# Performance work log

Hardware: AMD Instinct MI355X
Metric: run time of the kernel (lower is better)

The kernel has to match this reference:

```python
import jax, jax.numpy as jnp
import numpy as np

L_MAX = 3
N_RADIAL = [2, 2, 1, 1]  # radial powers r^{2k} with 2k+l <= l_max=3


def fibonacci_sphere(n):
    i = np.arange(n, dtype=np.float64)
    phi = np.pi * (3.0 - np.sqrt(5.0))
    y = 1.0 - 2.0 * i / (n - 1)
    r = np.sqrt(np.maximum(1.0 - y * y, 0.0))
    th = phi * i
    pts = np.stack([np.cos(th) * r, y, np.sin(th) * r], -1)
    return jnp.asarray(pts, dtype=jnp.float32)


def real_sh(u):
    # real spherical harmonics on unit vectors u[...,3], degrees 0..3
    x, y, z = u[..., 0], u[..., 1], u[..., 2]
    Y0 = 0.28209479 * jnp.ones_like(x)[..., None]
    Y1 = 0.48860251 * jnp.stack([y, z, x], -1)
    Y2 = jnp.stack([
        1.09254843 * x * y,
        1.09254843 * y * z,
        0.31539157 * (3.0 * z * z - 1.0),
        1.09254843 * x * z,
        0.54627421 * (x * x - y * y)], -1)
    Y3 = jnp.stack([
        0.59004359 * y * (3.0 * x * x - y * y),
        2.89061144 * x * y * z,
        0.45704579 * y * (5.0 * z * z - 1.0),
        0.37317633 * z * (5.0 * z * z - 3.0),
        0.45704579 * x * (5.0 * z * z - 1.0),
        1.44530572 * z * (x * x - y * y),
        0.59004359 * x * (x * x - 3.0 * y * y)], -1)
    return [Y0, Y1, Y2, Y3]


def grid_sample_3d(vol, grid):
    # vol: [B, D, H, W]; grid: [B, d, h, w, 3], grid[...,0]->W, [...,1]->H, [...,2]->D
    # align_corners=True, zeros padding (torch.nn.functional.grid_sample semantics)
    B, Dv, Hv, Wv = vol.shape
    ix = (grid[..., 0] + 1.0) * 0.5 * (Wv - 1)
    iy = (grid[..., 1] + 1.0) * 0.5 * (Hv - 1)
    iz = (grid[..., 2] + 1.0) * 0.5 * (Dv - 1)
    x0f, y0f, z0f = jnp.floor(ix), jnp.floor(iy), jnp.floor(iz)
    wx, wy, wz = ix - x0f, iy - y0f, iz - z0f
    x0, y0, z0 = x0f.astype(jnp.int32), y0f.astype(jnp.int32), z0f.astype(jnp.int32)
    x1, y1, z1 = x0 + 1, y0 + 1, z0 + 1
    bidx = jnp.arange(B).reshape(B, 1, 1, 1)

    def tap(zi, yi, xi):
        m = ((zi >= 0) & (zi < Dv) & (yi >= 0) & (yi < Hv) & (xi >= 0) & (xi < Wv)).astype(vol.dtype)
        v = vol[bidx, jnp.clip(zi, 0, Dv - 1), jnp.clip(yi, 0, Hv - 1), jnp.clip(xi, 0, Wv - 1)]
        return v * m

    out = (tap(z0, y0, x0) * (1 - wz) * (1 - wy) * (1 - wx)
         + tap(z0, y0, x1) * (1 - wz) * (1 - wy) * wx
         + tap(z0, y1, x0) * (1 - wz) * wy * (1 - wx)
         + tap(z0, y1, x1) * (1 - wz) * wy * wx
         + tap(z1, y0, x0) * wz * (1 - wy) * (1 - wx)
         + tap(z1, y0, x1) * wz * (1 - wy) * wx
         + tap(z1, y1, x0) * wz * wy * (1 - wx)
         + tap(z1, y1, x1) * wz * wy * wx)
    return out


def setup_inputs() -> dict:
    key = jax.random.key(0)
    ks = jax.random.split(key, 12)
    B, H, W, D, S = 8, 32, 32, 32, 64
    x = jax.random.normal(ks[0], (B, H, W, D, 3), jnp.float32) * 0.35
    x_density = jax.random.uniform(ks[1], (B, H, W, D), jnp.float32)
    F = jax.random.normal(ks[2], (B, S, 256), jnp.float32) * 0.1
    def lin(k, i, o):
        return jax.random.normal(k, (i, o), jnp.float32) / np.sqrt(i)
    return {
        'x': x, 'x_density': x_density, 'F': F,
        'S2': fibonacci_sphere(S),
        'bw1': lin(ks[3], 256, 64), 'bb1': jnp.zeros((64,), jnp.float32),
        'bw2': lin(ks[4], 64, 3), 'bb2': jnp.zeros((3,), jnp.float32),
        'cw1': lin(ks[5], 256, 128), 'cb1': jnp.zeros((128,), jnp.float32),
        'cw2': lin(ks[6], 128, 64), 'cb2': jnp.zeros((64,), jnp.float32),
        'iw': lin(ks[7], 128, 3), 'ib': jnp.zeros((3,), jnp.float32),
    }


def reference(x, x_density, F, S2, bw1, bb1, bw2, bb2, cw1, cb1, cw2, cb2, iw, ib):
    B, H, W, D, _ = x.shape
    S = S2.shape[0]
    quad = (4.0 * jnp.pi) / S  # sphere quadrature weight for fibonacci samples
    Ybase = real_sh(S2)  # list of [S, 2l+1]

    # frame (E) branch: basis MLP -> type-1 SH coefficients -> normalize
    basis = jax.nn.relu(F @ bw1 + bb1) @ bw2 + bb2          # [B,S,3]
    E = jnp.einsum('vm,bvc->bmc', Ybase[1], basis) * quad   # [B,3,3]
    E = E / jnp.clip(jnp.linalg.norm(E, axis=-1, keepdims=True), 1e-6)

    # latent code branch: code MLP -> full SHT coefficients per degree l
    latent = jax.nn.relu(F @ cw1 + cb1) @ cw2 + cb2         # [B,S,64]
    coeffs = [jnp.einsum('vm,bvc->bmc', Ybase[l], latent) * quad for l in range(L_MAX + 1)]

    # zernike monomials of the grid points
    xf = x.reshape(B, -1, 3)                                # [B,V,3]
    r = jnp.linalg.norm(xf, axis=-1, keepdims=True)         # [B,V,1]
    u = xf / jnp.clip(r, 1e-6)
    Yx = real_sh(u)
    points_code = []
    points_inv = None
    for l in range(L_MAX + 1):
        Pl = Yx[l] * (r ** l)                               # solid harmonic [B,V,2l+1]
        rad = jnp.stack([r[..., 0] ** (2 * k) for k in range(N_RADIAL[l])], -1)  # [B,V,n_l]
        zl = Pl[..., :, None] * rad[..., None, :]           # [B,V,2l+1,n_l]
        p = jnp.einsum('bmi,bvmj->bvij', coeffs[l], zl)     # [B,V,64,n_l]
        p = p.reshape(B, p.shape[1], -1)
        points_code.append(p)
        if l == 1:
            points_inv = p                                  # [B,V,128]
    points_code = jnp.concatenate(points_code, -1)          # [B,V,384]

    pts = points_inv @ iw + ib                              # [B,V,3]
    coords = pts.reshape(B, H, W, D, 3)
    vol = x_density.reshape(B, H, W, D)
    sampled = grid_sample_3d(vol, coords)                   # [B,H,W,D]
    return sampled, E, coords, points_code
```

## Files before the change

kernel.cpp:

```cpp
#include <hip/hip_runtime.h>
#include <math.h>

#define OFF_E     262144
#define OFF_COORD 262216
#define OFF_CODE  1048648

#define QUAD 0.19634954084936207f

#define WS_H1 0
#define WS_H2 32768
#define WS_C  98304
#define WS_AB 106496

__global__ __launch_bounds__(384) void k_hidden(
    const float* __restrict__ F,
    const float* __restrict__ bw1, const float* __restrict__ bb1,
    const float* __restrict__ cw1, const float* __restrict__ cb1,
    float* __restrict__ ws)
{
    __shared__ float sF[8 * 257];
    const int blk = blockIdx.x;
    const int b   = blk >> 3;
    const int r0  = (blk & 7) * 8;
    const int tid = threadIdx.x;

    float* wsH1 = ws + WS_H1;
    float* wsH2 = ws + WS_H2;

    const float* Fb = F + ((size_t)b * 64 + r0) * 256;
    for (int i = tid; i < 2048; i += 384) sF[(i >> 8) * 257 + (i & 255)] = Fb[i];
    __syncthreads();

    if (tid < 128) {
        const int row = tid >> 4, k4 = (tid & 15) * 4;
        const float* fr = sF + row * 257;
        float4 acc = *(const float4*)&bb1[k4];
        #pragma unroll 4
        for (int j = 0; j < 256; ++j) {
            const float  f = fr[j];
            const float4 w = *(const float4*)&bw1[j * 64 + k4];
            acc.x = fmaf(f, w.x, acc.x);
            acc.y = fmaf(f, w.y, acc.y);
            acc.z = fmaf(f, w.z, acc.z);
            acc.w = fmaf(f, w.w, acc.w);
        }
        acc.x = fmaxf(acc.x, 0.f); acc.y = fmaxf(acc.y, 0.f);
        acc.z = fmaxf(acc.z, 0.f); acc.w = fmaxf(acc.w, 0.f);
        *(float4*)&wsH1[((size_t)b * 64 + r0 + row) * 64 + k4] = acc;
    } else {
        const int tt  = tid - 128;
        const int row = tt >> 5, k4 = (tt & 31) * 4;
        const float* fr = sF + row * 257;
        float4 acc = *(const float4*)&cb1[k4];
        #pragma unroll 4
        for (int j = 0; j < 256; ++j) {
            const float  f = fr[j];
            const float4 w = *(const float4*)&cw1[j * 128 + k4];
            acc.x = fmaf(f, w.x, acc.x);
            acc.y = fmaf(f, w.y, acc.y);
            acc.z = fmaf(f, w.z, acc.z);
            acc.w = fmaf(f, w.w, acc.w);
        }
        acc.x = fmaxf(acc.x, 0.f); acc.y = fmaxf(acc.y, 0.f);
        acc.z = fmaxf(acc.z, 0.f); acc.w = fmaxf(acc.w, 0.f);
        *(float4*)&wsH2[((size_t)b * 64 + r0 + row) * 128 + k4] = acc;
    }
}

__global__ __launch_bounds__(512) void k_coeffs(
    const float* __restrict__ ws_in,
    const float* __restrict__ S2,
    const float* __restrict__ bw2, const float* __restrict__ bb2,
    const float* __restrict__ cw2, const float* __restrict__ cb2,
    const float* __restrict__ iw,
    float* __restrict__ ws_out, float* __restrict__ outE)
{
    __shared__ float sH2[64 * 129];
    __shared__ alignas(16) float sLat[64 * 64];
    __shared__ float sY[64 * 16];
    __shared__ float sBas[64 * 3];
    __shared__ float sC[16 * 64];
    __shared__ float sE[9];

    const int b = blockIdx.x, tid = threadIdx.x;
    const float* wsH1 = ws_in + WS_H1;
    const float* wsH2 = ws_in + WS_H2;
    float* wsC  = ws_out + WS_C;
    float* wsAB = ws_out + WS_AB;

    const float* H2b = wsH2 + (size_t)b * 8192;
    for (int i = tid; i < 8192; i += 512) sH2[(i >> 7) * 129 + (i & 127)] = H2b[i];

    if (tid < 64) {
        const float x = S2[tid * 3 + 0], y = S2[tid * 3 + 1], z = S2[tid * 3 + 2];
        float* Yv = sY + tid * 16;
        Yv[0]  = 0.28209479f;
        Yv[1]  = 0.48860251f * y;
        Yv[2]  = 0.48860251f * z;
        Yv[3]  = 0.48860251f * x;
        Yv[4]  = 1.09254843f * x * y;
        Yv[5]  = 1.09254843f * y * z;
        Yv[6]  = 0.31539157f * (3.f * z * z - 1.f);
        Yv[7]  = 1.09254843f * x * z;
        Yv[8]  = 0.54627421f * (x * x - y * y);
        Yv[9]  = 0.59004359f * y * (3.f * x * x - y * y);
        Yv[10] = 2.89061144f * x * y * z;
        Yv[11] = 0.45704579f * y * (5.f * z * z - 1.f);
        Yv[12] = 0.37317633f * z * (5.f * z * z - 3.f);
        Yv[13] = 0.45704579f * x * (5.f * z * z - 1.f);
        Yv[14] = 1.44530572f * z * (x * x - y * y);
        Yv[15] = 0.59004359f * x * (x * x - 3.f * y * y);
    }

    float breg = 0.f;
    if (tid < 192) {
        const int v = tid / 3, c = tid % 3;
        const float* h1 = wsH1 + ((size_t)b * 64 + v) * 64;
        float acc = bb2[c];
        #pragma unroll 8
        for (int k = 0; k < 64; ++k) acc = fmaf(h1[k], bw2[k * 3 + c], acc);
        breg = acc;
    }
    __syncthreads();

    if (tid < 192) sBas[tid] = breg;

    for (int t = tid; t < 1024; t += 512) {
        const int row = t >> 4, i4 = (t & 15) * 4;
        const float* h2 = sH2 + row * 129;
        float4 acc = *(const float4*)&cb2[i4];
        #pragma unroll 4
        for (int k = 0; k < 128; ++k) {
            const float  h = h2[k];
            const float4 w = *(const float4*)&cw2[k * 64 + i4];
            acc.x = fmaf(h, w.x, acc.x);
            acc.y = fmaf(h, w.y, acc.y);
            acc.z = fmaf(h, w.z, acc.z);
            acc.w = fmaf(h, w.w, acc.w);
        }
        *(float4*)&sLat[row * 64 + i4] = acc;
    }
    __syncthreads();

    for (int o = tid; o < 1024; o += 512) {
        const int m = o >> 6, i = o & 63;
        float acc = 0.f;
        #pragma unroll 8
        for (int v = 0; v < 64; ++v) acc = fmaf(sY[v * 16 + m], sLat[v * 64 + i], acc);
        acc *= QUAD;
        sC[o] = acc;
        wsC[(size_t)b * 1024 + o] = acc;
    }
    if (tid < 9) {
        const int m = tid / 3, c = tid % 3;
        float acc = 0.f;
        for (int v = 0; v < 64; ++v) acc = fmaf(sY[v * 16 + 1 + m], sBas[v * 3 + c], acc);
        sE[tid] = acc * QUAD;
    }
    __syncthreads();

    if (tid < 9) {
        const int m = tid / 3;
        const float e0 = sE[m * 3 + 0], e1 = sE[m * 3 + 1], e2 = sE[m * 3 + 2];
        const float n = sqrtf(e0 * e0 + e1 * e1 + e2 * e2);
        outE[b * 9 + tid] = sE[tid] / fmaxf(n, 1e-6f);
    }
    if (tid < 18) {
        const int which = tid / 9, mc = tid % 9;
        const int m = mc / 3, c = mc % 3;
        float acc = 0.f;
        #pragma unroll 8
        for (int i = 0; i < 64; ++i)
            acc = fmaf(sC[(1 + m) * 64 + i], iw[(2 * i + which) * 3 + c], acc);
        wsAB[b * 18 + tid] = acc;
    }
}

__global__ __launch_bounds__(384) void k_points(
    const float* __restrict__ x, const float* __restrict__ dens,
    const float* __restrict__ ws, const float* __restrict__ ib,
    float* __restrict__ out)
{
    __shared__ alignas(16) float sC[16 * 64];
    __shared__ float sAB[18];
    __shared__ alignas(16) float sZ[128 * 20];

    const int blk = blockIdx.x;
    const int b   = blk >> 8;
    const int v0  = (blk & 255) * 128;
    const int tid = threadIdx.x;

    const float* wsC  = ws + WS_C;
    const float* wsAB = ws + WS_AB;

    if (tid < 256) ((float4*)sC)[tid] = ((const float4*)(wsC + (size_t)b * 1024))[tid];
    if (tid < 18) sAB[tid] = wsAB[b * 18 + tid];

    float z1 = 0.f, z2 = 0.f, z3 = 0.f, r2 = 0.f;
    size_t g = 0;
    if (tid < 128) {
        const int v = v0 + tid;
        g = (size_t)b * 32768 + v;
        const float px = x[g * 3 + 0], py = x[g * 3 + 1], pz = x[g * 3 + 2];
        r2 = px * px + py * py + pz * pz;
        const float r   = sqrtf(r2);
        const float inv = 1.f / fmaxf(r, 1e-6f);
        const float ux = px * inv, uy = py * inv, uz = pz * inv;
        float* Z = sZ + tid * 20;
        z1 = 0.48860251f * uy * r;
        z2 = 0.48860251f * uz * r;
        z3 = 0.48860251f * ux * r;
        Z[0] = z1; Z[1] = z2; Z[2] = z3; Z[3] = r2;
        const float r3 = r2 * r;
        Z[4]  = 0.59004359f * uy * (3.f * ux * ux - uy * uy) * r3;
        Z[5]  = 2.89061144f * ux * uy * uz * r3;
        Z[6]  = 0.45704579f * uy * (5.f * uz * uz - 1.f) * r3;
        Z[7]  = 0.37317633f * uz * (5.f * uz * uz - 3.f) * r3;
        Z[8]  = 0.45704579f * ux * (5.f * uz * uz - 1.f) * r3;
        Z[9]  = 1.44530572f * uz * (ux * ux - uy * uy) * r3;
        Z[10] = 0.59004359f * ux * (ux * ux - 3.f * uy * uy) * r3;
        Z[12] = 1.09254843f * ux * uy * r2;
        Z[13] = 1.09254843f * uy * uz * r2;
        Z[14] = 0.31539157f * (3.f * uz * uz - 1.f) * r2;
        Z[15] = 1.09254843f * ux * uz * r2;
        Z[16] = 0.54627421f * (ux * ux - uy * uy) * r2;
    }
    __syncthreads();

    const int c = tid;
    float* po = out + OFF_CODE + ((size_t)b * 32768 + v0) * 384 + c;
    if (c < 128) {
        const float cr = sC[c >> 1] * 0.28209479f;
        const bool  jr = (c & 1) != 0;
        #pragma unroll 4
        for (int v = 0; v < 128; ++v) {
            const float r2v = sZ[v * 20 + 3];
            const float a = jr ? cr * r2v : cr;
            po[(size_t)v * 384] = a;
        }
    } else if (c < 256) {
        const int  i  = (c - 128) >> 1;
        const bool jr = (c & 1) != 0;
        const float c0 = sC[1 * 64 + i], c1 = sC[2 * 64 + i], c2 = sC[3 * 64 + i];
        #pragma unroll 4
        for (int v = 0; v < 128; ++v) {
            const float4 z = *(const float4*)(sZ + v * 20);
            float a = c0 * z.x;
            a = fmaf(c1, z.y, a);
            a = fmaf(c2, z.z, a);
            a = jr ? a * z.w : a;
            po[(size_t)v * 384] = a;
        }
    } else if (c < 320) {
        const int i = c - 256;
        const float c0 = sC[4 * 64 + i], c1 = sC[5 * 64 + i], c2 = sC[6 * 64 + i];
        const float c3 = sC[7 * 64 + i], c4 = sC[8 * 64 + i];
        #pragma unroll 4
        for (int v = 0; v < 128; ++v) {
            const float4 z  = *(const float4*)(sZ + v * 20 + 12);
            const float  z4 = sZ[v * 20 + 16];
            float a = c0 * z.x;
            a = fmaf(c1, z.y, a);
            a = fmaf(c2, z.z, a);
            a = fmaf(c3, z.w, a);
            a = fmaf(c4, z4,  a);
            po[(size_t)v * 384] = a;
        }
    } else {
        const int i = c - 320;
        const float c0 = sC[ 9 * 64 + i], c1 = sC[10 * 64 + i], c2 = sC[11 * 64 + i];
        const float c3 = sC[12 * 64 + i], c4 = sC[13 * 64 + i], c5 = sC[14 * 64 + i];
        const float c6 = sC[15 * 64 + i];
        #pragma unroll 4
        for (int v = 0; v < 128; ++v) {
            const float4 za = *(const float4*)(sZ + v * 20 + 4);
            const float2 zb = *(const float2*)(sZ + v * 20 + 8);
            const float  zc = sZ[v * 20 + 10];
            float a = c0 * za.x;
            a = fmaf(c1, za.y, a);
            a = fmaf(c2, za.z, a);
            a = fmaf(c3, za.w, a);
            a = fmaf(c4, zb.x, a);
            a = fmaf(c5, zb.y, a);
            a = fmaf(c6, zc,  a);
            po[(size_t)v * 384] = a;
        }
    }

    if (tid < 128) {
        const float zr0 = z1, zr1 = z2, zr2 = z3;
        float pt[3];
        #pragma unroll
        for (int cc = 0; cc < 3; ++cc) {
            float acc = ib[cc];
            acc = fmaf(zr0, sAB[0 * 3 + cc] + r2 * sAB[9 + 0 * 3 + cc], acc);
            acc = fmaf(zr1, sAB[1 * 3 + cc] + r2 * sAB[9 + 1 * 3 + cc], acc);
            acc = fmaf(zr2, sAB[2 * 3 + cc] + r2 * sAB[9 + 2 * 3 + cc], acc);
            pt[cc] = acc;
            out[OFF_COORD + g * 3 + cc] = acc;
        }

        const float ix = (pt[0] + 1.f) * 0.5f * 31.f;
        const float iy = (pt[1] + 1.f) * 0.5f * 31.f;
        const float iz = (pt[2] + 1.f) * 0.5f * 31.f;
        const float x0f = floorf(ix), y0f = floorf(iy), z0f = floorf(iz);
        const float wx = ix - x0f, wy = iy - y0f, wz = iz - z0f;
        const int x0 = (int)x0f, y0 = (int)y0f, z0 = (int)z0f;
        const float* volb = dens + (size_t)b * 32768;
        float s = 0.f;
        #pragma unroll
        for (int dz = 0; dz < 2; ++dz) {
            const int zi = z0 + dz;
            const float wzz = dz ? wz : 1.f - wz;
            #pragma unroll
            for (int dy = 0; dy < 2; ++dy) {
                const int yi = y0 + dy;
                const float wyy = dy ? wy : 1.f - wy;
                #pragma unroll
                for (int dx = 0; dx < 2; ++dx) {
                    const int xi = x0 + dx;
                    const float wxx = dx ? wx : 1.f - wx;
                    if (zi >= 0 && zi < 32 && yi >= 0 && yi < 32 && xi >= 0 && xi < 32)
                        s += wzz * wyy * wxx * volb[zi * 1024 + yi * 32 + xi];
                }
            }
        }
        out[g] = s;
    }
}

extern "C" void kernel_launch(void* const* d_in, const int* in_sizes, int n_in,
                              void* d_out, int out_size, void* d_ws, size_t ws_size,
                              hipStream_t stream) {
    const float* x    = (const float*)d_in[0];
    const float* dens = (const float*)d_in[1];
    const float* F    = (const float*)d_in[2];
    const float* S2   = (const float*)d_in[3];
    const float* bw1  = (const float*)d_in[4];
    const float* bb1  = (const float*)d_in[5];
    const float* bw2  = (const float*)d_in[6];
    const float* bb2  = (const float*)d_in[7];
    const float* cw1  = (const float*)d_in[8];
    const float* cb1  = (const float*)d_in[9];
    const float* cw2  = (const float*)d_in[10];
    const float* cb2  = (const float*)d_in[11];
    const float* iw   = (const float*)d_in[12];
    const float* ib   = (const float*)d_in[13];
    float* out = (float*)d_out;
    float* ws  = (float*)d_ws;

    k_hidden<<<64,   384, 0, stream>>>(F, bw1, bb1, cw1, cb1, ws);
    k_coeffs<<<8,    512, 0, stream>>>(ws, S2, bw2, bb2, cw2, cb2, iw, ws, out + OFF_E);
    k_points<<<2048, 384, 0, stream>>>(x, dens, ws, ib, out);
}
```

Before: 588.0 us.

## Write points_code with float4 stores by remapping threads to column groups

Restructures the output stage of the points_code kernel so each thread computes four adjacent output columns for a quarter of the vertex rows and writes them as one float4 store. Previously each thread wrote one scalar column across all 128 rows. The goal is wider, more efficient global stores for the large code output, which is likely the dominant memory traffic. The cost is more registers per thread for coefficient arrays and a different per-wave write pattern, and the l=2 and l=3 sections now use only 64 threads each with four columns apiece.

```diff
diff --git a/kernel.cpp b/kernel.cpp
--- a/kernel.cpp
+++ b/kernel.cpp
@@ -227,63 +227,95 @@
     }
     __syncthreads();
 
-    const int c = tid;
-    float* po = out + OFF_CODE + ((size_t)b * 32768 + v0) * 384 + c;
-    if (c < 128) {
-        const float cr = sC[c >> 1] * 0.28209479f;
-        const bool  jr = (c & 1) != 0;
-        #pragma unroll 4
-        for (int v = 0; v < 128; ++v) {
-            const float r2v = sZ[v * 20 + 3];
-            const float a = jr ? cr * r2v : cr;
-            po[(size_t)v * 384] = a;
-        }
-    } else if (c < 256) {
-        const int  i  = (c - 128) >> 1;
-        const bool jr = (c & 1) != 0;
-        const float c0 = sC[1 * 64 + i], c1 = sC[2 * 64 + i], c2 = sC[3 * 64 + i];
-        #pragma unroll 4
-        for (int v = 0; v < 128; ++v) {
-            const float4 z = *(const float4*)(sZ + v * 20);
-            float a = c0 * z.x;
-            a = fmaf(c1, z.y, a);
-            a = fmaf(c2, z.z, a);
-            a = jr ? a * z.w : a;
-            po[(size_t)v * 384] = a;
-        }
-    } else if (c < 320) {
-        const int i = c - 256;
-        const float c0 = sC[4 * 64 + i], c1 = sC[5 * 64 + i], c2 = sC[6 * 64 + i];
-        const float c3 = sC[7 * 64 + i], c4 = sC[8 * 64 + i];
-        #pragma unroll 4
-        for (int v = 0; v < 128; ++v) {
-            const float4 z  = *(const float4*)(sZ + v * 20 + 12);
-            const float  z4 = sZ[v * 20 + 16];
-            float a = c0 * z.x;
-            a = fmaf(c1, z.y, a);
-            a = fmaf(c2, z.z, a);
-            a = fmaf(c3, z.w, a);
-            a = fmaf(c4, z4,  a);
-            po[(size_t)v * 384] = a;
+    const size_t rowbase = OFF_CODE + ((size_t)b * 32768 + v0) * 384;
+    if (tid < 128) {
+        const int q = tid & 31, vh = tid >> 5;
+        const float ca = sC[2 * q]     * 0.28209479f;
+        const float cb = sC[2 * q + 1] * 0.28209479f;
+        const float* zr = sZ + (vh * 32) * 20 + 3;
+        float* po = out + rowbase + (size_t)(vh * 32) * 384 + 4 * q;
+        #pragma unroll 4
+        for (int vi = 0; vi < 32; ++vi) {
+            const float r2v = zr[(size_t)vi * 20];
+            float4 o;
+            o.x = ca; o.y = ca * r2v; o.z = cb; o.w = cb * r2v;
+            *(float4*)po = o;
+            po += 384;
+        }
+    } else if (tid < 256) {
+        const int u = tid - 128, q = u & 31, vh = u >> 5;
+        const float c00 = sC[64 + 2 * q],     c01 = sC[128 + 2 * q],     c02 = sC[192 + 2 * q];
+        const float c10 = sC[64 + 2 * q + 1], c11 = sC[128 + 2 * q + 1], c12 = sC[192 + 2 * q + 1];
+        const float* zr = sZ + (vh * 32) * 20;
+        float* po = out + rowbase + (size_t)(vh * 32) * 384 + 128 + 4 * q;
+        #pragma unroll 4
+        for (int vi = 0; vi < 32; ++vi) {
+            const float4 z = *(const float4*)(zr + (size_t)vi * 20);
+            float d0 = c00 * z.x; d0 = fmaf(c01, z.y, d0); d0 = fmaf(c02, z.z, d0);
+            float d1 = c10 * z.x; d1 = fmaf(c11, z.y, d1); d1 = fmaf(c12, z.z, d1);
+            float4 o;
+            o.x = d0; o.y = d0 * z.w; o.z = d1; o.w = d1 * z.w;
+            *(float4*)po = o;
+            po += 384;
+        }
+    } else if (tid < 320) {
+        const int ln = tid & 63, q = ln & 15, vh = ln >> 4;
+        const int i0 = 4 * q;
+        float cf[5][4];
+        #pragma unroll
+        for (int m = 0; m < 5; ++m)
+            #pragma unroll
+            for (int k = 0; k < 4; ++k) cf[m][k] = sC[(4 + m) * 64 + i0 + k];
+        const float* zr = sZ + (vh * 32) * 20;
+        float* po = out + rowbase + (size_t)(vh * 32) * 384 + 256 + i0;
+        #pragma unroll 4
+        for (int vi = 0; vi < 32; ++vi) {
+            const float4 za = *(const float4*)(zr + (size_t)vi * 20 + 12);
+            const float  zb = zr[(size_t)vi * 20 + 16];
+            float4 o;
+            float* a = &o.x;
+            #pragma unroll
+            for (int k = 0; k < 4; ++k) {
+                float acc = cf[0][k] * za.x;
+                acc = fmaf(cf[1][k], za.y, acc);
+                acc = fmaf(cf[2][k], za.z, acc);
+                acc = fmaf(cf[3][k], za.w, acc);
+                acc = fmaf(cf[4][k], zb,   acc);
+                a[k] = acc;
+            }
+            *(float4*)po = o;
+            po += 384;
         }
     } else {
-        const int i = c - 320;
-        const float c0 = sC[ 9 * 64 + i], c1 = sC[10 * 64 + i], c2 = sC[11 * 64 + i];
-        const float c3 = sC[12 * 64 + i], c4 = sC[13 * 64 + i], c5 = sC[14 * 64 + i];
-        const float c6 = sC[15 * 64 + i];
-        #pragma unroll 4
-        for (int v = 0; v < 128; ++v) {
-            const float4 za = *(const float4*)(sZ + v * 20 + 4);
-            const float2 zb = *(const float2*)(sZ + v * 20 + 8);
-            const float  zc = sZ[v * 20 + 10];
-            float a = c0 * za.x;
-            a = fmaf(c1, za.y, a);
-            a = fmaf(c2, za.z, a);
-            a = fmaf(c3, za.w, a);
-            a = fmaf(c4, zb.x, a);
-            a = fmaf(c5, zb.y, a);
-            a = fmaf(c6, zc,  a);
-            po[(size_t)v * 384] = a;
+        const int ln = tid & 63, q = ln & 15, vh = ln >> 4;
+        const int i0 = 4 * q;
+        float cf[7][4];
+        #pragma unroll
+        for (int m = 0; m < 7; ++m)
+            #pragma unroll
+            for (int k = 0; k < 4; ++k) cf[m][k] = sC[(9 + m) * 64 + i0 + k];
+        const float* zr = sZ + (vh * 32) * 20;
+        float* po = out + rowbase + (size_t)(vh * 32) * 384 + 320 + i0;
+        #pragma unroll 2
+        for (int vi = 0; vi < 32; ++vi) {
+            const float4 za = *(const float4*)(zr + (size_t)vi * 20 + 4);
+            const float2 zb = *(const float2*)(zr + (size_t)vi * 20 + 8);
+            const float  zc = zr[(size_t)vi * 20 + 10];
+            float4 o;
+            float* a = &o.x;
+            #pragma unroll
+            for (int k = 0; k < 4; ++k) {
+                float acc = cf[0][k] * za.x;
+                acc = fmaf(cf[1][k], za.y, acc);
+                acc = fmaf(cf[2][k], za.z, acc);
+                acc = fmaf(cf[3][k], za.w, acc);
+                acc = fmaf(cf[4][k], zb.x, acc);
+                acc = fmaf(cf[5][k], zb.y, acc);
+                acc = fmaf(cf[6][k], zc,   acc);
+                a[k] = acc;
+            }
+            *(float4*)po = o;
+            po += 384;
         }
     }
 
```

Result: faster. 556.5 us (-5.4%).

## Restructure point-code kernel for vectorized float4 stores and smaller blocks

Applied to the files above, without the earlier changes.

The points kernel is rewritten so each thread produces four consecutive code channels and writes them with a single 16-byte vector store. It uses a padded per-point monomial table in shared memory with uniform per-segment coefficient vectors, instead of one scalar store per thread per point. Blocks now cover 64 points (4096 blocks) with a batch-interleaved block index, and the coordinate and grid-sample work runs on 64 threads before the sync. This targets the store throughput of the large 384-wide code output, at the cost of some redundant multiplies by zero padding.

```diff
diff --git a/kernel.cpp b/kernel.cpp
--- a/kernel.cpp
+++ b/kernel.cpp
@@ -11,6 +11,8 @@
 #define WS_H2 32768
 #define WS_C  98304
 #define WS_AB 106496
+
+typedef float f4v __attribute__((ext_vector_type(4)));
 
 __global__ __launch_bounds__(384) void k_hidden(
     const float* __restrict__ F,
@@ -176,135 +178,74 @@
     }
 }
 
-__global__ __launch_bounds__(384) void k_points(
+__global__ __launch_bounds__(384) void k_code(
     const float* __restrict__ x, const float* __restrict__ dens,
     const float* __restrict__ ws, const float* __restrict__ ib,
     float* __restrict__ out)
 {
-    __shared__ alignas(16) float sC[16 * 64];
-    __shared__ float sAB[18];
-    __shared__ alignas(16) float sZ[128 * 20];
-
-    const int blk = blockIdx.x;
-    const int b   = blk >> 8;
-    const int v0  = (blk & 255) * 128;
-    const int tid = threadIdx.x;
-
-    const float* wsC  = ws + WS_C;
-    const float* wsAB = ws + WS_AB;
-
-    if (tid < 256) ((float4*)sC)[tid] = ((const float4*)(wsC + (size_t)b * 1024))[tid];
-    if (tid < 18) sAB[tid] = wsAB[b * 18 + tid];
-
-    float z1 = 0.f, z2 = 0.f, z3 = 0.f, r2 = 0.f;
-    size_t g = 0;
-    if (tid < 128) {
-        const int v = v0 + tid;
-        g = (size_t)b * 32768 + v;
-        const float px = x[g * 3 + 0], py = x[g * 3 + 1], pz = x[g * 3 + 2];
-        r2 = px * px + py * py + pz * pz;
+    __shared__ alignas(16) float sC[1024];
+    __shared__ alignas(16) float sT[64 * 32];
+
+    const int blk   = blockIdx.x;
+    const int b     = blk & 7;
+    const int vbase = (blk >> 3) * 64;
+    const int tid   = threadIdx.x;
+
+    if (tid < 256)
+        ((f4v*)sC)[tid] = ((const f4v*)(ws + WS_C + b * 1024))[tid];
+
+    if (tid < 64) {
+        const int g = b * 32768 + vbase + tid;
+        const float px = x[(size_t)g * 3 + 0];
+        const float py = x[(size_t)g * 3 + 1];
+        const float pz = x[(size_t)g * 3 + 2];
+        const float r2 = px * px + py * py + pz * pz;
         const float r   = sqrtf(r2);
         const float inv = 1.f / fmaxf(r, 1e-6f);
         const float ux = px * inv, uy = py * inv, uz = pz * inv;
-        float* Z = sZ + tid * 20;
-        z1 = 0.48860251f * uy * r;
-        z2 = 0.48860251f * uz * r;
-        z3 = 0.48860251f * ux * r;
-        Z[0] = z1; Z[1] = z2; Z[2] = z3; Z[3] = r2;
         const float r3 = r2 * r;
-        Z[4]  = 0.59004359f * uy * (3.f * ux * ux - uy * uy) * r3;
-        Z[5]  = 2.89061144f * ux * uy * uz * r3;
-        Z[6]  = 0.45704579f * uy * (5.f * uz * uz - 1.f) * r3;
-        Z[7]  = 0.37317633f * uz * (5.f * uz * uz - 3.f) * r3;
-        Z[8]  = 0.45704579f * ux * (5.f * uz * uz - 1.f) * r3;
-        Z[9]  = 1.44530572f * uz * (ux * ux - uy * uy) * r3;
-        Z[10] = 0.59004359f * ux * (ux * ux - 3.f * uy * uy) * r3;
-        Z[12] = 1.09254843f * ux * uy * r2;
-        Z[13] = 1.09254843f * uy * uz * r2;
-        Z[14] = 0.31539157f * (3.f * uz * uz - 1.f) * r2;
-        Z[15] = 1.09254843f * ux * uz * r2;
-        Z[16] = 0.54627421f * (ux * ux - uy * uy) * r2;
-    }
-    __syncthreads();
-
-    const int c = tid;
-    float* po = out + OFF_CODE + ((size_t)b * 32768 + v0) * 384 + c;
-    if (c < 128) {
-        const float cr = sC[c >> 1] * 0.28209479f;
-        const bool  jr = (c & 1) != 0;
-        #pragma unroll 4
-        for (int v = 0; v < 128; ++v) {
-            const float r2v = sZ[v * 20 + 3];
-            const float a = jr ? cr * r2v : cr;
-            po[(size_t)v * 384] = a;
-        }
-    } else if (c < 256) {
-        const int  i  = (c - 128) >> 1;
-        const bool jr = (c & 1) != 0;
-        const float c0 = sC[1 * 64 + i], c1 = sC[2 * 64 + i], c2 = sC[3 * 64 + i];
-        #pragma unroll 4
-        for (int v = 0; v < 128; ++v) {
-            const float4 z = *(const float4*)(sZ + v * 20);
-            float a = c0 * z.x;
-            a = fmaf(c1, z.y, a);
-            a = fmaf(c2, z.z, a);
-            a = jr ? a * z.w : a;
-            po[(size_t)v * 384] = a;
-        }
-    } else if (c < 320) {
-        const int i = c - 256;
-        const float c0 = sC[4 * 64 + i], c1 = sC[5 * 64 + i], c2 = sC[6 * 64 + i];
-        const float c3 = sC[7 * 64 + i], c4 = sC[8 * 64 + i];
-        #pragma unroll 4
-        for (int v = 0; v < 128; ++v) {
-            const float4 z  = *(const float4*)(sZ + v * 20 + 12);
-            const float  z4 = sZ[v * 20 + 16];
-            float a = c0 * z.x;
-            a = fmaf(c1, z.y, a);
-            a = fmaf(c2, z.z, a);
-            a = fmaf(c3, z.w, a);
-            a = fmaf(c4, z4,  a);
-            po[(size_t)v * 384] = a;
-        }
-    } else {
-        const int i = c - 320;
-        const float c0 = sC[ 9 * 64 + i], c1 = sC[10 * 64 + i], c2 = sC[11 * 64 + i];
-        const float c3 = sC[12 * 64 + i], c4 = sC[13 * 64 + i], c5 = sC[14 * 64 + i];
-        const float c6 = sC[15 * 64 + i];
-        #pragma unroll 4
-        for (int v = 0; v < 128; ++v) {
-            const float4 za = *(const float4*)(sZ + v * 20 + 4);
-            const float2 zb = *(const float2*)(sZ + v * 20 + 8);
-            const float  zc = sZ[v * 20 + 10];
-            float a = c0 * za.x;
-            a = fmaf(c1, za.y, a);
-            a = fmaf(c2, za.z, a);
-            a = fmaf(c3, za.w, a);
-            a = fmaf(c4, zb.x, a);
-            a = fmaf(c5, zb.y, a);
-            a = fmaf(c6, zc,  a);
-            po[(size_t)v * 384] = a;
-        }
-    }
-
-    if (tid < 128) {
-        const float zr0 = z1, zr1 = z2, zr2 = z3;
+
+        const float z1 = 0.48860251f * uy * r;
+        const float z2 = 0.48860251f * uz * r;
+        const float z3 = 0.48860251f * ux * r;
+
+        float* T = sT + tid * 32;
+        T[0]  = 1.f;  T[1] = r2;  T[2] = 0.f; T[3] = 0.f;
+        T[4]  = 0.f;  T[5] = 0.f; T[6] = 0.f; T[7] = 0.f;
+        T[8]  = z1;   T[9] = z2;  T[10] = z3;
+        T[11] = z1 * r2; T[12] = z2 * r2; T[13] = z3 * r2;
+        T[14] = 0.f;  T[15] = 0.f;
+        T[16] = 1.09254843f * ux * uy * r2;
+        T[17] = 1.09254843f * uy * uz * r2;
+        T[18] = 0.31539157f * (3.f * uz * uz - 1.f) * r2;
+        T[19] = 1.09254843f * ux * uz * r2;
+        T[20] = 0.54627421f * (ux * ux - uy * uy) * r2;
+        T[21] = 0.f; T[22] = 0.f; T[23] = 0.f;
+        T[24] = 0.59004359f * uy * (3.f * ux * ux - uy * uy) * r3;
+        T[25] = 2.89061144f * ux * uy * uz * r3;
+        T[26] = 0.45704579f * uy * (5.f * uz * uz - 1.f) * r3;
+        T[27] = 0.37317633f * uz * (5.f * uz * uz - 3.f) * r3;
+        T[28] = 0.45704579f * ux * (5.f * uz * uz - 1.f) * r3;
+        T[29] = 1.44530572f * uz * (ux * ux - uy * uy) * r3;
+        T[30] = 0.59004359f * ux * (ux * ux - 3.f * uy * uy) * r3;
+        T[31] = 0.f;
+
+        const float* AB = ws + WS_AB + b * 18;
         float pt[3];
         #pragma unroll
         for (int cc = 0; cc < 3; ++cc) {
             float acc = ib[cc];
-            acc = fmaf(zr0, sAB[0 * 3 + cc] + r2 * sAB[9 + 0 * 3 + cc], acc);
-            acc = fmaf(zr1, sAB[1 * 3 + cc] + r2 * sAB[9 + 1 * 3 + cc], acc);
-            acc = fmaf(zr2, sAB[2 * 3 + cc] + r2 * sAB[9 + 2 * 3 + cc], acc);
+            acc = fmaf(z1, AB[0 + cc] + r2 * AB[9  + cc], acc);
+            acc = fmaf(z2, AB[3 + cc] + r2 * AB[12 + cc], acc);
+            acc = fmaf(z3, AB[6 + cc] + r2 * AB[15 + cc], acc);
             pt[cc] = acc;
-            out[OFF_COORD + g * 3 + cc] = acc;
-        }
-
-        const float ix = (pt[0] + 1.f) * 0.5f * 31.f;
-        const float iy = (pt[1] + 1.f) * 0.5f * 31.f;
-        const float iz = (pt[2] + 1.f) * 0.5f * 31.f;
-        const float x0f = floorf(ix), y0f = floorf(iy), z0f = floorf(iz);
-        const float wx = ix - x0f, wy = iy - y0f, wz = iz - z0f;
+            out[OFF_COORD + (size_t)g * 3 + cc] = acc;
+        }
+        const float ixf = (pt[0] + 1.f) * 0.5f * 31.f;
+        const float iyf = (pt[1] + 1.f) * 0.5f * 31.f;
+        const float izf = (pt[2] + 1.f) * 0.5f * 31.f;
+        const float x0f = floorf(ixf), y0f = floorf(iyf), z0f = floorf(izf);
+        const float wx = ixf - x0f, wy = iyf - y0f, wz = izf - z0f;
         const int x0 = (int)x0f, y0 = (int)y0f, z0 = (int)z0f;
         const float* volb = dens + (size_t)b * 32768;
         float s = 0.f;
@@ -327,6 +268,71 @@
         }
         out[g] = s;
     }
+    __syncthreads();
+
+    const int w  = tid >> 6, l = tid & 63;
+    const int g0 = w * 256 + 4 * l;
+    const int rw = g0 / 384;
+    const int c  = g0 - rw * 384;
+
+    f4v cf0 = {0.f,0.f,0.f,0.f}, cf1 = cf0, cf2 = cf0, cf3 = cf0;
+    f4v cf4 = cf0, cf5 = cf0, cf6 = cf0;
+    int tb;
+    if (c < 128) {
+        const int i0 = c >> 1;
+        const float ca = sC[i0]     * 0.28209479f;
+        const float cb = sC[i0 + 1] * 0.28209479f;
+        cf0 = (f4v){ca, 0.f, cb, 0.f};
+        cf1 = (f4v){0.f, ca, 0.f, cb};
+        tb = 0;
+    } else if (c < 256) {
+        const int u = (c - 128) >> 1;
+        const float a0 = sC[64 + u],     a1 = sC[128 + u],     a2 = sC[192 + u];
+        const float b0 = sC[64 + u + 1], b1 = sC[128 + u + 1], b2 = sC[192 + u + 1];
+        cf0 = (f4v){a0, 0.f, b0, 0.f};
+        cf1 = (f4v){a1, 0.f, b1, 0.f};
+        cf2 = (f4v){a2, 0.f, b2, 0.f};
+        cf3 = (f4v){0.f, a0, 0.f, b0};
+        cf4 = (f4v){0.f, a1, 0.f, b1};
+        cf5 = (f4v){0.f, a2, 0.f, b2};
+        tb = 8;
+    } else if (c < 320) {
+        const int i0 = c - 256;
+        cf0 = *(const f4v*)&sC[4 * 64 + i0];
+        cf1 = *(const f4v*)&sC[5 * 64 + i0];
+        cf2 = *(const f4v*)&sC[6 * 64 + i0];
+        cf3 = *(const f4v*)&sC[7 * 64 + i0];
+        cf4 = *(const f4v*)&sC[8 * 64 + i0];
+        tb = 16;
+    } else {
+        const int i0 = c - 320;
+        cf0 = *(const f4v*)&sC[ 9 * 64 + i0];
+        cf1 = *(const f4v*)&sC[10 * 64 + i0];
+        cf2 = *(const f4v*)&sC[11 * 64 + i0];
+        cf3 = *(const f4v*)&sC[12 * 64 + i0];
+        cf4 = *(const f4v*)&sC[13 * 64 + i0];
+        cf5 = *(const f4v*)&sC[14 * 64 + i0];
+        cf6 = *(const f4v*)&sC[15 * 64 + i0];
+        tb = 24;
+    }
+
+    const float* Tb = sT + tb;
+    float* po = out + OFF_CODE + ((size_t)(b * 32768 + vbase)) * 384 + g0;
+
+    #pragma unroll 4
+    for (int p = 0; p < 16; ++p) {
+        const int ro = (4 * p + rw) * 32;
+        const f4v ta = *(const f4v*)(Tb + ro);
+        const f4v tb4 = *(const f4v*)(Tb + ro + 4);
+        f4v acc = cf0 * ta.x;
+        acc += cf1 * ta.y;
+        acc += cf2 * ta.z;
+        acc += cf3 * ta.w;
+        acc += cf4 * tb4.x;
+        acc += cf5 * tb4.y;
+        acc += cf6 * tb4.z;
+        *(f4v*)(po + p * 1536) = acc;
+    }
 }
 
 extern "C" void kernel_launch(void* const* d_in, const int* in_sizes, int n_in,
@@ -351,5 +357,5 @@
 
     k_hidden<<<64,   384, 0, stream>>>(F, bw1, bb1, cw1, cb1, ws);
     k_coeffs<<<8,    512, 0, stream>>>(ws, S2, bw2, bb2, cw2, cb2, iw, ws, out + OFF_E);
-    k_points<<<2048, 384, 0, stream>>>(x, dens, ws, ib, out);
+    k_code<<<4096,   384, 0, stream>>>(x, dens, ws, ib, out);
 }
```

Result: faster. 503.6 us (-14.4%).
